# Performance work log

Measured on AMD Instinct MI355X. Metric: run time of the kernel, lower is better.

## Reference

```python
import jax, jax.numpy as jnp
import numpy as np

S, I, H, FC, O = 16384, 64, 1024, 128, 1


def setup_inputs() -> dict:
    key = jax.random.key(0)
    ks = jax.random.split(key, 9)
    s_lstm = 1.0 / np.sqrt(H)
    return {
        "input_seq": jax.random.normal(ks[0], (S, I), jnp.float32),
        "W_ih": jax.random.uniform(ks[1], (4 * H, I), jnp.float32, -s_lstm, s_lstm),
        "W_hh": jax.random.uniform(ks[2], (4 * H, H), jnp.float32, -s_lstm, s_lstm),
        "b_ih": jax.random.uniform(ks[3], (4 * H,), jnp.float32, -s_lstm, s_lstm),
        "b_hh": jax.random.uniform(ks[4], (4 * H,), jnp.float32, -s_lstm, s_lstm),
        "fc1_w": jax.random.uniform(ks[5], (FC, H), jnp.float32, -s_lstm, s_lstm),
        "fc1_b": jax.random.uniform(ks[6], (FC,), jnp.float32, -s_lstm, s_lstm),
        "fc2_w": jax.random.uniform(ks[7], (O, FC), jnp.float32, -1.0 / np.sqrt(FC), 1.0 / np.sqrt(FC)),
        "fc2_b": jax.random.uniform(ks[8], (O,), jnp.float32, -1.0 / np.sqrt(FC), 1.0 / np.sqrt(FC)),
    }


def _lstm_scan(x, W_ih, W_hh, b_ih, b_hh):
    # PyTorch gate order: i, f, g, o. batch=1 collapsed; x: [S, I]
    xg = x @ W_ih.T + (b_ih + b_hh)  # precompute input-side gates: [S, 4H]

    def step(carry, xg_t):
        h, c = carry
        gates = xg_t + h @ W_hh.T
        i, f, g, o = jnp.split(gates, 4)
        i = jax.nn.sigmoid(i)
        f = jax.nn.sigmoid(f)
        g = jnp.tanh(g)
        o = jax.nn.sigmoid(o)
        c = f * c + i * g
        h = o * jnp.tanh(c)
        return (h, c), h

    h0 = jnp.zeros((H,), x.dtype)
    c0 = jnp.zeros((H,), x.dtype)
    _, hs = jax.lax.scan(step, (h0, c0), xg)
    return hs  # [S, H]


def reference(input_seq, W_ih, W_hh, b_ih, b_hh, fc1_w, fc1_b, fc2_w, fc2_b):
    hs = _lstm_scan(input_seq, W_ih, W_hh, b_ih, b_hh)       # [S, H]
    x = jax.nn.relu(hs)                                       # relu on LSTM outputs
    x = jax.nn.relu(x @ fc1_w.T + fc1_b)                      # [S, 128]
    x = x @ fc2_w.T + fc2_b                                   # [S, 1]
    return x[-1]                                              # [1]
```

## Files before the change

### kernel.cpp

```cpp
#include <hip/hip_runtime.h>
#include <hip/hip_fp16.h>


#define S_LEN 16384
#define I_DIM 64
#define H_DIM 1024
#define NBLK  64
#define NTHR  1024

__device__ __forceinline__ float sigmoidf_(float x) { return 1.0f / (1.0f + __expf(-x)); }
__device__ __forceinline__ float tanh_fast(float x) { return 1.0f - 2.0f / (__expf(2.0f * x) + 1.0f); }

__global__ __launch_bounds__(NTHR, 4) void lstm_persistent(
    const float* __restrict__ xseq,
    const float* __restrict__ W_ih,
    const float* __restrict__ W_hh,
    const float* __restrict__ b_ih,
    const float* __restrict__ b_hh,
    unsigned* __restrict__ pairs)
{
    const int b   = blockIdx.x;
    const int tid = threadIdx.x;
    const int w   = tid >> 6;
    const int c   = tid & 63;
    const int g   = w >> 2;
    const int r0  = (w & 3) * 4;

    __shared__ float4 h_stage[H_DIM / 4];
    __shared__ float  x_stage[2][I_DIM];
    __shared__ float  gs[64];
    __shared__ float  bias_s[64];

    float4 wh[4][4];
    float  wi[4];
    #pragma unroll
    for (int q = 0; q < 4; ++q) {
        const int grow = g * H_DIM + 16 * b + r0 + q;
        const float4* wr = (const float4*)(W_hh + (size_t)grow * H_DIM);
        #pragma unroll
        for (int s = 0; s < 4; ++s) wh[q][s] = wr[s * 64 + c];
        wi[q] = W_ih[(size_t)grow * I_DIM + c];
    }
    if (tid < 64) {
        const int grow = (tid >> 4) * H_DIM + 16 * b + (tid & 15);
        bias_s[tid] = b_ih[grow] + b_hh[grow];
    }
    float cst = 0.0f;
    if (tid < H_DIM / 4) h_stage[tid] = make_float4(0.f, 0.f, 0.f, 0.f);
    if (tid < 16) ((float4*)x_stage[0])[tid] = ((const float4*)xseq)[tid];
    __syncthreads();

    for (int t = 0; t < S_LEN; ++t) {
        if (w == 14 && c < 16 && t + 1 < S_LEN)
            ((float4*)x_stage[(t + 1) & 1])[c] =
                ((const float4*)(xseq + (size_t)(t + 1) * I_DIM))[c];

        float acc[4] = {0.f, 0.f, 0.f, 0.f};
        #pragma unroll
        for (int s = 0; s < 4; ++s) {
            const float4 hv = h_stage[s * 64 + c];
            #pragma unroll
            for (int q = 0; q < 4; ++q) {
                acc[q] = fmaf(wh[q][s].x, hv.x, acc[q]);
                acc[q] = fmaf(wh[q][s].y, hv.y, acc[q]);
                acc[q] = fmaf(wh[q][s].z, hv.z, acc[q]);
                acc[q] = fmaf(wh[q][s].w, hv.w, acc[q]);
            }
        }
        {
            const float xv = x_stage[t & 1][c];
            #pragma unroll
            for (int q = 0; q < 4; ++q) acc[q] = fmaf(wi[q], xv, acc[q]);
        }
        #pragma unroll
        for (int q = 0; q < 4; ++q) {
            #pragma unroll
            for (int off = 32; off > 0; off >>= 1)
                acc[q] += __shfl_xor(acc[q], off, 64);
        }
        if (c == 0) {
            #pragma unroll
            for (int q = 0; q < 4; ++q) gs[g * 16 + r0 + q] = acc[q];
        }
        __syncthreads();

        if (tid < 16) {
            const float pi  = gs[tid]      + bias_s[tid];
            const float pfg = gs[16 + tid] + bias_s[16 + tid];
            const float pg  = gs[32 + tid] + bias_s[32 + tid];
            const float po  = gs[48 + tid] + bias_s[48 + tid];
            const float ig = sigmoidf_(pi);
            const float fg = sigmoidf_(pfg);
            const float gg = tanh_fast(pg);
            const float og = sigmoidf_(po);
            cst = fg * cst + ig * gg;
            const float h = og * tanh_fast(cst);
            const unsigned pk = ((unsigned)(t + 1) << 16) |
                                (unsigned)__half_as_ushort(__float2half(h));
            __hip_atomic_store(&pairs[(size_t)(t & 1) * H_DIM + 16 * b + tid], pk,
                               __ATOMIC_RELAXED, __HIP_MEMORY_SCOPE_AGENT);
        }

        if (t == S_LEN - 1) break;

        if (w == 15) {
            const unsigned long long* P =
                (const unsigned long long*)(pairs + (size_t)(t & 1) * H_DIM);
            const unsigned long long tag = (unsigned long long)(unsigned)(t + 1);
            const unsigned long long expv = (tag << 48) | (tag << 16);
            const unsigned long long msk  = 0xFFFF0000FFFF0000ull;
            unsigned long long v[8];
            for (;;) {
                bool ok = true;
                #pragma unroll
                for (int u = 0; u < 8; ++u) {
                    v[u] = __hip_atomic_load(P + 64 * u + c,
                                             __ATOMIC_RELAXED, __HIP_MEMORY_SCOPE_AGENT);
                    ok = ok && ((v[u] & msk) == expv);
                }
                if (ok) break;
            }
            float2* hs2 = (float2*)h_stage;
            #pragma unroll
            for (int u = 0; u < 8; ++u) {
                const float lo = __half2float(__ushort_as_half((unsigned short)(v[u] & 0xFFFFu)));
                const float hi = __half2float(__ushort_as_half((unsigned short)((v[u] >> 32) & 0xFFFFu)));
                hs2[64 * u + c] = make_float2(lo, hi);
            }
        }
        __syncthreads();
    }
}

__global__ __launch_bounds__(256) void fc_head(
    const unsigned* __restrict__ pairs,
    const float* __restrict__ fc1_w,
    const float* __restrict__ fc1_b,
    const float* __restrict__ fc2_w,
    const float* __restrict__ fc2_b,
    float* __restrict__ out)
{
    const int tid = threadIdx.x;
    __shared__ float4 hr4[H_DIM / 4];
    __shared__ float  partial[256];
    __shared__ float  r1[128];

    const uint4 pa = ((const uint4*)(pairs + H_DIM))[tid];
    float4 hv = make_float4(__half2float(__ushort_as_half((unsigned short)(pa.x & 0xFFFFu))),
                            __half2float(__ushort_as_half((unsigned short)(pa.y & 0xFFFFu))),
                            __half2float(__ushort_as_half((unsigned short)(pa.z & 0xFFFFu))),
                            __half2float(__ushort_as_half((unsigned short)(pa.w & 0xFFFFu))));
    hv.x = fmaxf(hv.x, 0.f); hv.y = fmaxf(hv.y, 0.f);
    hv.z = fmaxf(hv.z, 0.f); hv.w = fmaxf(hv.w, 0.f);
    hr4[tid] = hv;
    __syncthreads();

    const int row = tid & 127, half = tid >> 7;
    const float4* wrow = (const float4*)(fc1_w + (size_t)row * H_DIM) + half * 128;
    float a0 = 0.f, a1 = 0.f;
    #pragma unroll 4
    for (int i = 0; i < 128; i += 2) {
        const float4 w0 = wrow[i],     h0 = hr4[half * 128 + i];
        const float4 w1 = wrow[i + 1], h1 = hr4[half * 128 + i + 1];
        a0 += w0.x * h0.x + w0.y * h0.y + w0.z * h0.z + w0.w * h0.w;
        a1 += w1.x * h1.x + w1.y * h1.y + w1.z * h1.z + w1.w * h1.w;
    }
    partial[tid] = a0 + a1;
    __syncthreads();
    if (tid < 128) {
        const float s = partial[tid] + partial[tid + 128] + fc1_b[tid];
        r1[tid] = fmaxf(s, 0.f);
    }
    __syncthreads();
    if (tid < 64) {
        float v = r1[tid] * fc2_w[tid] + r1[tid + 64] * fc2_w[tid + 64];
        #pragma unroll
        for (int off = 32; off > 0; off >>= 1) v += __shfl_xor(v, off, 64);
        if (tid == 0) out[0] = v + fc2_b[0];
    }
}

extern "C" void kernel_launch(void* const* d_in, const int* in_sizes, int n_in,
                              void* d_out, int out_size, void* d_ws, size_t ws_size,
                              hipStream_t stream) {
    (void)in_sizes; (void)n_in; (void)out_size; (void)ws_size;
    const float* xseq  = (const float*)d_in[0];
    const float* W_ih  = (const float*)d_in[1];
    const float* W_hh  = (const float*)d_in[2];
    const float* b_ih  = (const float*)d_in[3];
    const float* b_hh  = (const float*)d_in[4];
    const float* fc1_w = (const float*)d_in[5];
    const float* fc1_b = (const float*)d_in[6];
    const float* fc2_w = (const float*)d_in[7];
    const float* fc2_b = (const float*)d_in[8];
    unsigned* pairs = (unsigned*)d_ws;

    lstm_persistent<<<NBLK, NTHR, 0, stream>>>(xseq, W_ih, W_hh, b_ih, b_hh, pairs);
    fc_head<<<1, 256, 0, stream>>>(pairs, fc1_w, fc1_b, fc2_w, fc2_b, (float*)d_out);
}
```

Before: 43.28 ms.

## Store recurrent weights as fp16 in registers and use fdot2 with 512 threads

Packs the W_hh weights into half2 registers so each block can run with 512 threads, each covering 8 gate rows, and computes the recurrent matvec with v_dot2 fp16 instructions against an h vector staged in shared memory as packed halves. The polling for the next h, which was done by a single wave, is now spread across all 512 threads, one 64-bit word each, with s_sleep between attempts, and each thread writes its packed pair straight into shared memory. This aims to shorten per-step latency with fewer instructions and a simpler gather. The cost is lower precision from fp16 weights, more shuffle reductions per thread, and more threads hitting global memory while they spin.

```diff
diff --git a/kernel.cpp b/kernel.cpp
--- a/kernel.cpp
+++ b/kernel.cpp
@@ -6,12 +6,18 @@
 #define I_DIM 64
 #define H_DIM 1024
 #define NBLK  64
-#define NTHR  1024
+#define NTHR  512
+
+typedef _Float16 half2_t __attribute__((ext_vector_type(2)));
 
 __device__ __forceinline__ float sigmoidf_(float x) { return 1.0f / (1.0f + __expf(-x)); }
 __device__ __forceinline__ float tanh_fast(float x) { return 1.0f - 2.0f / (__expf(2.0f * x) + 1.0f); }
-
-__global__ __launch_bounds__(NTHR, 4) void lstm_persistent(
+__device__ __forceinline__ unsigned pack2(float a, float b) {
+    return (unsigned)__half_as_ushort(__float2half(a)) |
+           ((unsigned)__half_as_ushort(__float2half(b)) << 16);
+}
+
+__global__ __launch_bounds__(NTHR, 2) void lstm_persistent(
     const float* __restrict__ xseq,
     const float* __restrict__ W_ih,
     const float* __restrict__ W_hh,
@@ -23,64 +29,73 @@
     const int tid = threadIdx.x;
     const int w   = tid >> 6;
     const int c   = tid & 63;
-    const int g   = w >> 2;
-    const int r0  = (w & 3) * 4;
-
-    __shared__ float4 h_stage[H_DIM / 4];
-    __shared__ float  x_stage[2][I_DIM];
-    __shared__ float  gs[64];
-    __shared__ float  bias_s[64];
-
-    float4 wh[4][4];
-    float  wi[4];
+
+    __shared__ unsigned h_stage[H_DIM / 2];
+    __shared__ float    x_stage[2][I_DIM];
+    __shared__ float    gs[64];
+    __shared__ float    bias_s[64];
+
+    unsigned wreg[8][8];
+    float    wi[8];
     #pragma unroll
-    for (int q = 0; q < 4; ++q) {
-        const int grow = g * H_DIM + 16 * b + r0 + q;
-        const float4* wr = (const float4*)(W_hh + (size_t)grow * H_DIM);
-        #pragma unroll
-        for (int s = 0; s < 4; ++s) wh[q][s] = wr[s * 64 + c];
-        wi[q] = W_ih[(size_t)grow * I_DIM + c];
-    }
+    for (int r = 0; r < 8; ++r) {
+        const int rr   = 8 * w + r;
+        const int grow = (rr >> 4) * H_DIM + 16 * b + (rr & 15);
+        const float4* base = (const float4*)(W_hh + (size_t)grow * H_DIM);
+        #pragma unroll
+        for (int s = 0; s < 4; ++s) {
+            const float4 f = base[s * 64 + c];
+            wreg[r][2 * s]     = pack2(f.x, f.y);
+            wreg[r][2 * s + 1] = pack2(f.z, f.w);
+        }
+        wi[r] = W_ih[(size_t)grow * I_DIM + c];
+    }
+    #pragma unroll
+    for (int r = 0; r < 8; ++r)
+        asm volatile("" : "+v"(wreg[r][0]), "+v"(wreg[r][1]), "+v"(wreg[r][2]),
+                          "+v"(wreg[r][3]), "+v"(wreg[r][4]), "+v"(wreg[r][5]),
+                          "+v"(wreg[r][6]), "+v"(wreg[r][7]));
+
     if (tid < 64) {
         const int grow = (tid >> 4) * H_DIM + 16 * b + (tid & 15);
         bias_s[tid] = b_ih[grow] + b_hh[grow];
     }
     float cst = 0.0f;
-    if (tid < H_DIM / 4) h_stage[tid] = make_float4(0.f, 0.f, 0.f, 0.f);
+    h_stage[tid] = 0u;
     if (tid < 16) ((float4*)x_stage[0])[tid] = ((const float4*)xseq)[tid];
     __syncthreads();
 
     for (int t = 0; t < S_LEN; ++t) {
-        if (w == 14 && c < 16 && t + 1 < S_LEN)
+        if (w == 7 && c < 16 && t + 1 < S_LEN)
             ((float4*)x_stage[(t + 1) & 1])[c] =
                 ((const float4*)(xseq + (size_t)(t + 1) * I_DIM))[c];
 
-        float acc[4] = {0.f, 0.f, 0.f, 0.f};
+        float acc[8] = {0.f, 0.f, 0.f, 0.f, 0.f, 0.f, 0.f, 0.f};
         #pragma unroll
         for (int s = 0; s < 4; ++s) {
-            const float4 hv = h_stage[s * 64 + c];
-            #pragma unroll
-            for (int q = 0; q < 4; ++q) {
-                acc[q] = fmaf(wh[q][s].x, hv.x, acc[q]);
-                acc[q] = fmaf(wh[q][s].y, hv.y, acc[q]);
-                acc[q] = fmaf(wh[q][s].z, hv.z, acc[q]);
-                acc[q] = fmaf(wh[q][s].w, hv.w, acc[q]);
+            const uint2 hv = *(const uint2*)&h_stage[s * 128 + 2 * c];
+            const half2_t ha = __builtin_bit_cast(half2_t, hv.x);
+            const half2_t hb = __builtin_bit_cast(half2_t, hv.y);
+            #pragma unroll
+            for (int r = 0; r < 8; ++r) {
+                acc[r] = __builtin_amdgcn_fdot2(__builtin_bit_cast(half2_t, wreg[r][2 * s]),     ha, acc[r], false);
+                acc[r] = __builtin_amdgcn_fdot2(__builtin_bit_cast(half2_t, wreg[r][2 * s + 1]), hb, acc[r], false);
             }
         }
         {
             const float xv = x_stage[t & 1][c];
             #pragma unroll
-            for (int q = 0; q < 4; ++q) acc[q] = fmaf(wi[q], xv, acc[q]);
-        }
-        #pragma unroll
-        for (int q = 0; q < 4; ++q) {
+            for (int r = 0; r < 8; ++r) acc[r] = fmaf(wi[r], xv, acc[r]);
+        }
+        #pragma unroll
+        for (int r = 0; r < 8; ++r) {
             #pragma unroll
             for (int off = 32; off > 0; off >>= 1)
-                acc[q] += __shfl_xor(acc[q], off, 64);
+                acc[r] += __shfl_xor(acc[r], off, 64);
         }
         if (c == 0) {
             #pragma unroll
-            for (int q = 0; q < 4; ++q) gs[g * 16 + r0 + q] = acc[q];
+            for (int r = 0; r < 8; ++r) gs[8 * w + r] = acc[r];
         }
         __syncthreads();
 
@@ -103,30 +118,18 @@
 
         if (t == S_LEN - 1) break;
 
-        if (w == 15) {
+        {
             const unsigned long long* P =
                 (const unsigned long long*)(pairs + (size_t)(t & 1) * H_DIM);
-            const unsigned long long tag = (unsigned long long)(unsigned)(t + 1);
+            const unsigned long long tag  = (unsigned long long)(unsigned)(t + 1);
             const unsigned long long expv = (tag << 48) | (tag << 16);
-            const unsigned long long msk  = 0xFFFF0000FFFF0000ull;
-            unsigned long long v[8];
+            unsigned long long v;
             for (;;) {
-                bool ok = true;
-                #pragma unroll
-                for (int u = 0; u < 8; ++u) {
-                    v[u] = __hip_atomic_load(P + 64 * u + c,
-                                             __ATOMIC_RELAXED, __HIP_MEMORY_SCOPE_AGENT);
-                    ok = ok && ((v[u] & msk) == expv);
-                }
-                if (ok) break;
+                v = __hip_atomic_load(P + tid, __ATOMIC_RELAXED, __HIP_MEMORY_SCOPE_AGENT);
+                if ((v & 0xFFFF0000FFFF0000ull) == expv) break;
+                __builtin_amdgcn_s_sleep(1);
             }
-            float2* hs2 = (float2*)h_stage;
-            #pragma unroll
-            for (int u = 0; u < 8; ++u) {
-                const float lo = __half2float(__ushort_as_half((unsigned short)(v[u] & 0xFFFFu)));
-                const float hi = __half2float(__ushort_as_half((unsigned short)((v[u] >> 32) & 0xFFFFu)));
-                hs2[64 * u + c] = make_float2(lo, hi);
-            }
+            h_stage[tid] = (unsigned)(v & 0xFFFFu) | (((unsigned)(v >> 32) & 0xFFFFu) << 16);
         }
         __syncthreads();
     }
```

After: 41.11 ms. 1.05x faster.
